# Performance work log

Hardware: AMD Instinct MI355X
Metric: run time of the kernel (lower is better)

The kernel has to match this reference:

```python
import jax, jax.numpy as jnp
import numpy as np

N = 50000      # n_nodes
E = 800000     # directed edges (symmetric set, no self-loops)
D_IN = 128
D_HID = 128
EPS = 1e-5     # LayerNorm eps (torch default)


def setup_inputs() -> dict:
    rng = np.random.default_rng(0)
    a = rng.integers(0, N, 700000, dtype=np.int64)
    b = rng.integers(0, N, 700000, dtype=np.int64)
    m = a != b
    a, b = a[m], b[m]
    # symmetric, deduplicated edge set (no self-loops); shuffle before truncation
    keys = np.unique(np.concatenate([a * N + b, b * N + a]))
    keys = rng.permutation(keys)[:E]
    row = (keys // N).astype(np.int32)
    col = (keys % N).astype(np.int32)
    ks = jax.random.split(jax.random.key(0), 6)
    return {
        "x": jax.random.normal(ks[0], (N, D_IN), jnp.float32),
        "W0": jax.random.normal(ks[1], (D_IN, D_HID), jnp.float32) / np.float32(np.sqrt(D_IN)),
        "b0": jnp.zeros((D_HID,), jnp.float32),
        "W1": jax.random.normal(ks[2], (D_HID, D_HID), jnp.float32) / np.float32(np.sqrt(D_HID)),
        "b1": jnp.zeros((D_HID,), jnp.float32),
        "ln1_g": jnp.ones((D_HID,), jnp.float32),
        "ln1_b": jnp.zeros((D_HID,), jnp.float32),
        "ln2_g": jnp.ones((D_HID,), jnp.float32),
        "ln2_b": jnp.zeros((D_HID,), jnp.float32),
        "drop_W": jax.random.normal(ks[3], (1, 2), jnp.float32) * 10.0,
        "drop_b": jnp.zeros((1,), jnp.float32),
        "row": jnp.asarray(row),
        "col": jnp.asarray(col),
    }


def _layernorm(h, g, b):
    mu = jnp.mean(h, axis=-1, keepdims=True)
    var = jnp.var(h, axis=-1, keepdims=True)
    return (h - mu) * jax.lax.rsqrt(var + EPS) * g + b


def _att_coef(h, row, col, drop_W, drop_b):
    # fused on-device version of the CPU att_coef: per-edge cosine sim,
    # threshold, row-l1-normalize, learned binary drop, self-loop lam, exp.
    n = h.shape[0]
    norms = jnp.sqrt(jnp.sum(h * h, axis=1))                      # [n]
    sim = jnp.sum(h[row] * h[col], axis=1) / (norms[row] * norms[col])  # [E]
    sim = jnp.where(sim < 0.1, 0.0, sim)
    rs = jax.ops.segment_sum(sim, row, num_segments=n)            # row l1 norms
    att = sim / jnp.where(rs[row] > 0, rs[row], 1.0)
    # reverse-edge lookup att[col,row] via sorted uint32 keys (n*n < 2**32)
    nn = jnp.uint32(n)
    keys = row.astype(jnp.uint32) * nn + col.astype(jnp.uint32)
    order = jnp.argsort(keys)
    sk = keys[order]
    rk = col.astype(jnp.uint32) * nn + row.astype(jnp.uint32)
    pos = jnp.clip(jnp.searchsorted(sk, rk), 0, keys.shape[0] - 1)
    att_rev = jnp.where(sk[pos] == rk, att[order[pos]], 0.0)
    # drop_learn: Linear(2,1) -> sigmoid -> Threshold(0.5,0) -> Threshold(-0.49,1)
    # net effect: binary mask = 1 if sigmoid(score) > 0.5 else 0
    score = jax.nn.sigmoid(att * drop_W[0, 0] + att_rev * drop_W[0, 1] + drop_b[0])
    att = att * (score > 0.5).astype(h.dtype)
    deg = jax.ops.segment_sum((att != 0).astype(h.dtype), row, num_segments=n)
    lam = 1.0 / (deg + 1.0)                                       # self-loop weight
    w_e = jnp.where(att != 0, jnp.exp(att), 0.0)                  # exp only on stored nnz
    w_diag = jnp.exp(lam)
    # original computes attention on CPU numpy -> detached from autograd
    return jax.lax.stop_gradient(w_e), jax.lax.stop_gradient(w_diag)


def _conv(h, w_e, w_diag, row, col, W, b):
    s = h @ W                                                      # [n, d_out]
    agg = jax.ops.segment_sum(w_e[:, None] * s[col], row, num_segments=h.shape[0])
    return agg + w_diag[:, None] * s + b


def reference(x, W0, b0, W1, b1, ln1_g, ln1_b, ln2_g, ln2_b, drop_W, drop_b, row, col):
    h = x
    # layer 0
    w_e, w_d = _att_coef(h, row, col, drop_W, drop_b)
    h = _conv(h, w_e, w_d, row, col, W0, b0)
    h = jax.nn.relu(_layernorm(h, ln1_g, ln1_b))   # dropout: eval mode -> identity
    # layer 1
    w_e, w_d = _att_coef(h, row, col, drop_W, drop_b)
    h = _conv(h, w_e, w_d, row, col, W1, b1)
    h = jax.nn.relu(_layernorm(h, ln2_g, ln2_b))
    # final block: source bug reuses the last loop conv (convs[-2] == W1,b1)
    w_e, w_d = _att_coef(h, row, col, drop_W, drop_b)
    h = _conv(h, w_e, w_d, row, col, W1, b1)
    return jax.nn.log_softmax(h, axis=-1)
```

## Files before the change

kernel.cpp:

```cpp
#include <hip/hip_runtime.h>
#include <hip/hip_bf16.h>

#define D 128
#define EPS 1e-5f
#define SCAP 32

__global__ __launch_bounds__(256) void k_pre(
    const int* __restrict__ row, int* __restrict__ cnt, int E,
    const float* __restrict__ h, float* __restrict__ nrm, int N, int cB) {
  if ((int)blockIdx.x < cB) {
    int e = blockIdx.x * 256 + threadIdx.x;
    if (e < E) atomicAdd(&cnt[row[e]], 1);
  } else {
    int i = (blockIdx.x - cB) * 8 + (threadIdx.x >> 5);
    int sub = threadIdx.x & 31;
    if (i >= N) return;
    float4 a = ((const float4*)(h + (size_t)i * D))[sub];
    float v = a.x * a.x + a.y * a.y + a.z * a.z + a.w * a.w;
    for (int off = 16; off > 0; off >>= 1) v += __shfl_down(v, off, 32);
    if (sub == 0) nrm[i] = sqrtf(v);
  }
}

__global__ __launch_bounds__(256) void k_bsum(const int* __restrict__ cnt,
                                              int* __restrict__ bsum) {
  int t = threadIdx.x;
  int base = blockIdx.x * 1024 + t * 4;
  int4 c4 = ((const int4*)(cnt + base))[0];
  int s = c4.x + c4.y + c4.z + c4.w;
  for (int off = 32; off > 0; off >>= 1) s += __shfl_down(s, off);
  __shared__ int sh[4];
  if ((t & 63) == 0) sh[t >> 6] = s;
  __syncthreads();
  if (t == 0) bsum[blockIdx.x] = sh[0] + sh[1] + sh[2] + sh[3];
}

__global__ __launch_bounds__(256) void k_bscan(const int* __restrict__ bsum,
                                               int* __restrict__ boff, int nb,
                                               int* __restrict__ rptr, int N, int E) {
  __shared__ int sh[256];
  int t = threadIdx.x;
  int v = (t < nb) ? bsum[t] : 0;
  sh[t] = v;
  __syncthreads();
  for (int off = 1; off < 256; off <<= 1) {
    int u = (t >= off) ? sh[t - off] : 0;
    __syncthreads();
    sh[t] += u;
    __syncthreads();
  }
  if (t < nb) boff[t] = sh[t] - v;
  if (t == 0) rptr[N] = E;
}

__global__ __launch_bounds__(256) void k_apply(const int* __restrict__ cnt,
                                               const int* __restrict__ boff,
                                               int* __restrict__ rptr, int N) {
  __shared__ int sh[256];
  int t = threadIdx.x;
  int base = blockIdx.x * 1024 + t * 4;
  int4 c4 = ((const int4*)(cnt + base))[0];
  int e1 = c4.x, e2 = c4.x + c4.y, e3 = c4.x + c4.y + c4.z;
  int tot = e3 + c4.w;
  sh[t] = tot;
  __syncthreads();
  for (int off = 1; off < 256; off <<= 1) {
    int u = (t >= off) ? sh[t - off] : 0;
    __syncthreads();
    sh[t] += u;
    __syncthreads();
  }
  int o = sh[t] - tot + boff[blockIdx.x];
  if (base + 0 < N) rptr[base + 0] = o;
  if (base + 1 < N) rptr[base + 1] = o + e1;
  if (base + 2 < N) rptr[base + 2] = o + e2;
  if (base + 3 < N) rptr[base + 3] = o + e3;
}

__global__ __launch_bounds__(256) void k_scatter(
    const int* __restrict__ row, const int* __restrict__ col,
    const int* __restrict__ rptr, int* __restrict__ cur,
    int* __restrict__ rowS, int* __restrict__ colS, int E) {
  int e = blockIdx.x * 256 + threadIdx.x;
  if (e < E) {
    int r = row[e];
    int p = rptr[r] + atomicAdd(&cur[r], 1);
    rowS[p] = r;
    colS[p] = col[e];
  }
}

__global__ __launch_bounds__(256) void k_rev(const int* __restrict__ rowS,
                                             const int* __restrict__ colS,
                                             const int* __restrict__ rptr,
                                             int* __restrict__ rev, int E) {
  int p = blockIdx.x * 256 + threadIdx.x;
  if (p >= E) return;
  int r = rowS[p], c = colS[p];
  int q1 = rptr[c + 1];
  int rv = -1;
  for (int q = rptr[c]; q < q1; ++q)
    if (colS[q] == r) { rv = q; break; }
  rev[p] = rv;
}

__global__ __launch_bounds__(256) void k_sim(
    const float* __restrict__ h, const float* __restrict__ nrm,
    const int* __restrict__ rptr, const int* __restrict__ colS,
    const int* __restrict__ rev, float* __restrict__ simS, int N) {
  __shared__ int cL[8 * SCAP];
  __shared__ int pL[8 * SCAP];
  __shared__ int rL[8 * SCAP];
  __shared__ float nL[8 * SCAP];
  int grp = threadIdx.x >> 5;
  int sub = threadIdx.x & 31;
  int half = grp & 1;
  int i = blockIdx.x * 8 + grp;
  if (i >= N) return;
  int gb = grp * SCAP;
  int p0 = rptr[i], p1 = rptr[i + 1];
  float4 ai = ((const float4*)(h + (size_t)i * D))[sub];
  float ni = nrm[i];
  for (int base = p0; base < p1; base += SCAP) {
    int p = base + sub;
    bool inr = p < p1;
    int c = inr ? colS[p] : 0;
    int rv = inr ? rev[p] : 0;
    bool ok = inr && (c > i || rv < 0);
    unsigned long long mb = __ballot(ok);
    unsigned mh = (unsigned)(mb >> (half * 32));
    int pos = __popc(mh & ((1u << sub) - 1u));
    int K = __popc(mh);
    if (ok) {
      cL[gb + pos] = c;
      pL[gb + pos] = p;
      rL[gb + pos] = rv;
      nL[gb + pos] = nrm[c];
    }
    __builtin_amdgcn_wave_barrier();
    for (int j0 = 0; j0 < K; j0 += 8) {
      int cc_[8];
      bool vv[8];
      float4 b[8];
#pragma unroll
      for (int k = 0; k < 8; ++k) {
        int idx = j0 + k;
        vv[k] = idx < K;
        cc_[k] = vv[k] ? cL[gb + idx] : i;
      }
#pragma unroll
      for (int k = 0; k < 8; ++k)
        b[k] = ((const float4*)(h + (size_t)cc_[k] * D))[sub];
#pragma unroll
      for (int k = 0; k < 8; ++k) {
        float v = ai.x * b[k].x + ai.y * b[k].y + ai.z * b[k].z + ai.w * b[k].w;
        for (int off = 16; off > 0; off >>= 1) v += __shfl_down(v, off, 32);
        if (sub == 0 && vv[k]) {
          int idx = j0 + k;
          float sm = v / (ni * nL[gb + idx]);
          sm = (sm < 0.1f) ? 0.0f : sm;
          simS[pL[gb + idx]] = sm;
          int rv2 = rL[gb + idx];
          if (rv2 >= 0) simS[rv2] = sm;
        }
      }
    }
    __builtin_amdgcn_wave_barrier();
  }
}

__global__ __launch_bounds__(256) void k_rs(const float* __restrict__ simS,
                                            const int* __restrict__ rptr,
                                            float* __restrict__ rsE, int N) {
  int i = blockIdx.x * 256 + threadIdx.x;
  if (i >= N) return;
  int p1 = rptr[i + 1];
  float rs = 0.f;
  for (int p = rptr[i]; p < p1; ++p) rs += simS[p];
  rsE[i] = (rs > 0.f) ? rs : 1.f;
}

__global__ __launch_bounds__(256) void k_gemm(const float* __restrict__ h,
                                              const float* __restrict__ W,
                                              float* __restrict__ S, int N) {
  __shared__ float Ws[64 * D];
  int t = threadIdx.x;
  int i0 = blockIdx.x * 64;
  int tx = t & 15, ty = t >> 4;
  int gi[4];
  bool vld[4];
#pragma unroll
  for (int r = 0; r < 4; ++r) {
    gi[r] = i0 + ty * 4 + r;
    vld[r] = gi[r] < N;
  }
  float acc[4][8] = {};
  for (int ph = 0; ph < 2; ++ph) {
    __syncthreads();
    for (int ch = 0; ch < 8; ++ch) {
      int q = t + 256 * ch;
      ((float4*)Ws)[q] = ((const float4*)(W + (size_t)ph * 64 * D))[q];
    }
    __syncthreads();
    for (int kk = 0; kk < 16; ++kk) {
      float4 a4[4];
#pragma unroll
      for (int r = 0; r < 4; ++r)
        a4[r] = vld[r] ? ((const float4*)(h + (size_t)gi[r] * D))[ph * 16 + kk]
                       : make_float4(0.f, 0.f, 0.f, 0.f);
      float4 b0[4], b1[4];
#pragma unroll
      for (int k = 0; k < 4; ++k) {
        b0[k] = ((const float4*)(Ws + (kk * 4 + k) * D))[tx];
        b1[k] = ((const float4*)(Ws + (kk * 4 + k) * D))[16 + tx];
      }
#pragma unroll
      for (int r = 0; r < 4; ++r) {
        float4 a = a4[r];
#pragma unroll
        for (int c = 0; c < 4; ++c) {
          acc[r][c] += a.x * (&b0[0].x)[c] + a.y * (&b0[1].x)[c] +
                       a.z * (&b0[2].x)[c] + a.w * (&b0[3].x)[c];
          acc[r][4 + c] += a.x * (&b1[0].x)[c] + a.y * (&b1[1].x)[c] +
                           a.z * (&b1[2].x)[c] + a.w * (&b1[3].x)[c];
        }
      }
    }
  }
#pragma unroll
  for (int r = 0; r < 4; ++r) {
    if (vld[r]) {
      ((float4*)(S + (size_t)gi[r] * D))[tx] =
          make_float4(acc[r][0], acc[r][1], acc[r][2], acc[r][3]);
      ((float4*)(S + (size_t)gi[r] * D))[16 + tx] =
          make_float4(acc[r][4], acc[r][5], acc[r][6], acc[r][7]);
    }
  }
}

template <int MODE>
__global__ __launch_bounds__(256) void k_combine(
    const float* __restrict__ s, const float* __restrict__ simS,
    const float* __restrict__ rsE, const int* __restrict__ rev,
    const int* __restrict__ rptr, const int* __restrict__ colS,
    const float* __restrict__ bias, const float* __restrict__ g,
    const float* __restrict__ be, const float* __restrict__ dWp,
    const float* __restrict__ dbp, float* __restrict__ outF,
    float* __restrict__ nrmOut, int N) {
  __shared__ float wL[8 * 32];
  __shared__ int cLd[8 * 32];
  int grp = threadIdx.x >> 5, sub = threadIdx.x & 31;
  int half = grp & 1;
  int i = blockIdx.x * 8 + grp;
  if (i >= N) return;
  int gb = grp * 32;
  float w0 = dWp[0], w1 = dWp[1], bd = dbp[0];
  int p0 = rptr[i], p1 = rptr[i + 1];
  float ri = rsE[i];
  float4 acc = make_float4(0.f, 0.f, 0.f, 0.f);
  int deg = 0;
  for (int base = p0; base < p1; base += 32) {
    int p = base + sub;
    bool inr = p < p1;
    float sm = inr ? simS[p] : 0.f;
    int c = inr ? colS[p] : 0;
    int rv = inr ? rev[p] : -1;
    bool keep = false;
    float a = 0.f;
    if (sm != 0.f) {
      a = sm / ri;
      float ar = (rv >= 0) ? sm / rsE[c] : 0.f;
      float x = a * w0 + ar * w1 + bd;
      float sc = (x >= 0.f) ? 1.f / (1.f + expf(-x)) : expf(x) / (1.f + expf(x));
      keep = sc > 0.5f;
    }
    unsigned long long mb = __ballot(keep);
    unsigned mh = (unsigned)(mb >> (half * 32));
    int pos = __popc(mh & ((1u << sub) - 1u));
    int K = __popc(mh);
    if (keep) {
      wL[gb + pos] = expf(a);
      cLd[gb + pos] = c;
    }
    __builtin_amdgcn_wave_barrier();
    deg += K;
    for (int j0 = 0; j0 < K; j0 += 8) {
      int cc_[8];
      float ww[8];
      float4 b[8];
#pragma unroll
      for (int k = 0; k < 8; ++k) {
        int idx = j0 + k;
        bool vv = idx < K;
        cc_[k] = vv ? cLd[gb + idx] : i;
        ww[k] = vv ? wL[gb + idx] : 0.f;
      }
#pragma unroll
      for (int k = 0; k < 8; ++k)
        b[k] = ((const float4*)(s + (size_t)cc_[k] * D))[sub];
#pragma unroll
      for (int k = 0; k < 8; ++k) {
        acc.x += ww[k] * b[k].x; acc.y += ww[k] * b[k].y;
        acc.z += ww[k] * b[k].z; acc.w += ww[k] * b[k].w;
      }
    }
    __builtin_amdgcn_wave_barrier();
  }
  float wd = expf(1.0f / (float)(deg + 1));
  float4 sv = ((const float4*)(s + (size_t)i * D))[sub];
  float4 bb = ((const float4*)bias)[sub];
  float4 v = make_float4(acc.x + wd * sv.x + bb.x, acc.y + wd * sv.y + bb.y,
                         acc.z + wd * sv.z + bb.z, acc.w + wd * sv.w + bb.w);
  if (MODE == 0) {
    float sm = v.x + v.y + v.z + v.w;
    for (int off = 16; off > 0; off >>= 1) sm += __shfl_down(sm, off, 32);
    float mu = __shfl(sm, 0, 32) * (1.f / 128.f);
    float4 dv = make_float4(v.x - mu, v.y - mu, v.z - mu, v.w - mu);
    float q = dv.x * dv.x + dv.y * dv.y + dv.z * dv.z + dv.w * dv.w;
    for (int off = 16; off > 0; off >>= 1) q += __shfl_down(q, off, 32);
    float var = __shfl(q, 0, 32) * (1.f / 128.f);
    float rstd = rsqrtf(var + EPS);
    float4 gg = ((const float4*)g)[sub];
    float4 eb = ((const float4*)be)[sub];
    float4 y = make_float4(fmaxf(dv.x * rstd * gg.x + eb.x, 0.f),
                           fmaxf(dv.y * rstd * gg.y + eb.y, 0.f),
                           fmaxf(dv.z * rstd * gg.z + eb.z, 0.f),
                           fmaxf(dv.w * rstd * gg.w + eb.w, 0.f));
    ((float4*)(outF + (size_t)i * D))[sub] = y;
    float q2 = y.x * y.x + y.y * y.y + y.z * y.z + y.w * y.w;
    for (int off = 16; off > 0; off >>= 1) q2 += __shfl_down(q2, off, 32);
    if (sub == 0) nrmOut[i] = sqrtf(q2);
  } else {
    float mx = fmaxf(fmaxf(v.x, v.y), fmaxf(v.z, v.w));
    for (int off = 16; off > 0; off >>= 1) mx = fmaxf(mx, __shfl_down(mx, off, 32));
    float m = __shfl(mx, 0, 32);
    float es = expf(v.x - m) + expf(v.y - m) + expf(v.z - m) + expf(v.w - m);
    for (int off = 16; off > 0; off >>= 1) es += __shfl_down(es, off, 32);
    float l = logf(__shfl(es, 0, 32)) + m;
    ((float4*)(outF + (size_t)i * D))[sub] =
        make_float4(v.x - l, v.y - l, v.z - l, v.w - l);
  }
}

extern "C" void kernel_launch(void* const* d_in, const int* in_sizes, int n_in,
                              void* d_out, int out_size, void* d_ws, size_t ws_size,
                              hipStream_t stream) {
  const float* x   = (const float*)d_in[0];
  const float* W0  = (const float*)d_in[1];
  const float* b0  = (const float*)d_in[2];
  const float* W1  = (const float*)d_in[3];
  const float* b1  = (const float*)d_in[4];
  const float* g1  = (const float*)d_in[5];
  const float* be1 = (const float*)d_in[6];
  const float* g2  = (const float*)d_in[7];
  const float* be2 = (const float*)d_in[8];
  const float* dW  = (const float*)d_in[9];
  const float* db  = (const float*)d_in[10];
  const int* row   = (const int*)d_in[11];
  const int* col   = (const int*)d_in[12];
  int N = in_sizes[0] / D;
  int E = in_sizes[11];
  float* out = (float*)d_out;

  float* base = (float*)d_ws;
  size_t off = 0;
  auto alloc = [&](size_t elems) {
    float* p = base + off;
    off += (elems + 3) & ~(size_t)3;
    return p;
  };
  size_t N128 = (size_t)N * D;
  int nb = (N + 1023) / 1024;
  int NpadS = nb * 1024;
  float* hA   = alloc(N128);
  float* hB   = alloc(N128);
  float* s    = alloc(N128);
  int*   rowS = (int*)alloc(E);
  int*   colS = (int*)alloc(E);
  int*   rev  = (int*)alloc(E);
  float* simS = alloc(E);
  int*   cc   = (int*)alloc((size_t)2 * NpadS);
  int*   cnt  = cc;
  int*   cur  = cc + NpadS;
  int*   rptr = (int*)alloc(N + 1);
  float* rsE  = alloc(N);
  float* nrm  = alloc(N);
  int*   bsum = (int*)alloc(nb);
  int*   boff = (int*)alloc(nb);
  (void)ws_size; (void)n_in; (void)out_size;

  int cB = (E + 255) / 256;
  int nB = (N + 7) / 8;
  int nG = (N + 63) / 64;
  int nSim = (N + 7) / 8;
  int nRs = (N + 255) / 256;
  int nC = (N + 7) / 8;

  hipMemsetAsync(cc, 0, (size_t)2 * NpadS * sizeof(int), stream);
  k_pre<<<cB + nB, 256, 0, stream>>>(row, cnt, E, x, nrm, N, cB);
  k_bsum<<<nb, 256, 0, stream>>>(cnt, bsum);
  k_bscan<<<1, 256, 0, stream>>>(bsum, boff, nb, rptr, N, E);
  k_apply<<<nb, 256, 0, stream>>>(cnt, boff, rptr, N);
  k_scatter<<<cB, 256, 0, stream>>>(row, col, rptr, cur, rowS, colS, E);
  k_rev<<<cB, 256, 0, stream>>>(rowS, colS, rptr, rev, E);

  auto layer = [&](const float* hin, float* hout, const float* Wf,
                   const float* bf, const float* gf, const float* bef,
                   float* nrmOut, int mode) {
    k_sim<<<nSim, 256, 0, stream>>>(hin, nrm, rptr, colS, rev, simS, N);
    k_rs<<<nRs, 256, 0, stream>>>(simS, rptr, rsE, N);
    k_gemm<<<nG, 256, 0, stream>>>(hin, Wf, s, N);
    if (mode == 0)
      k_combine<0><<<nC, 256, 0, stream>>>(s, simS, rsE, rev, rptr, colS, bf, gf,
                                           bef, dW, db, hout, nrmOut, N);
    else
      k_combine<1><<<nC, 256, 0, stream>>>(s, simS, rsE, rev, rptr, colS, bf, gf,
                                           bef, dW, db, hout, nullptr, N);
  };
  layer(x, hA, W0, b0, g1, be1, nrm, 0);
  layer(hA, hB, W1, b1, g2, be2, nrm, 0);
  layer(hB, out, W1, b1, nullptr, nullptr, nullptr, 1);
}
```

Measured before the change: 612.9 us.

## Merge similarity and GEMM kernels into one launch; drop rowS array

The per-edge cosine-similarity kernel and the dense h@W GEMM are combined into a single launch, with block index selecting the role, so both run concurrently instead of back to back. The reverse-edge search kernel now maps one 32-lane group per row, which removes the need for the sorted row array and its writes. The combined kernel always reserves 32KB of shared memory for the GEMM tile, even in similarity blocks, which may lower occupancy for the similarity part.

```diff
diff --git a/kernel.cpp b/kernel.cpp
--- a/kernel.cpp
+++ b/kernel.cpp
@@ -80,92 +80,151 @@
 __global__ __launch_bounds__(256) void k_scatter(
     const int* __restrict__ row, const int* __restrict__ col,
     const int* __restrict__ rptr, int* __restrict__ cur,
-    int* __restrict__ rowS, int* __restrict__ colS, int E) {
+    int* __restrict__ colS, int E) {
   int e = blockIdx.x * 256 + threadIdx.x;
   if (e < E) {
     int r = row[e];
     int p = rptr[r] + atomicAdd(&cur[r], 1);
-    rowS[p] = r;
     colS[p] = col[e];
   }
 }
 
-__global__ __launch_bounds__(256) void k_rev(const int* __restrict__ rowS,
-                                             const int* __restrict__ colS,
+__global__ __launch_bounds__(256) void k_rev(const int* __restrict__ colS,
                                              const int* __restrict__ rptr,
-                                             int* __restrict__ rev, int E) {
-  int p = blockIdx.x * 256 + threadIdx.x;
-  if (p >= E) return;
-  int r = rowS[p], c = colS[p];
-  int q1 = rptr[c + 1];
-  int rv = -1;
-  for (int q = rptr[c]; q < q1; ++q)
-    if (colS[q] == r) { rv = q; break; }
-  rev[p] = rv;
-}
-
-__global__ __launch_bounds__(256) void k_sim(
+                                             int* __restrict__ rev, int N) {
+  int grp = threadIdx.x >> 5, sub = threadIdx.x & 31;
+  int i = blockIdx.x * 8 + grp;
+  if (i >= N) return;
+  int p0 = rptr[i], p1 = rptr[i + 1];
+  for (int p = p0 + sub; p < p1; p += 32) {
+    int c = colS[p];
+    int q1 = rptr[c + 1];
+    int rv = -1;
+    for (int q = rptr[c]; q < q1; ++q)
+      if (colS[q] == i) { rv = q; break; }
+    rev[p] = rv;
+  }
+}
+
+__global__ __launch_bounds__(256) void k_simgemm(
     const float* __restrict__ h, const float* __restrict__ nrm,
     const int* __restrict__ rptr, const int* __restrict__ colS,
-    const int* __restrict__ rev, float* __restrict__ simS, int N) {
+    const int* __restrict__ rev, float* __restrict__ simS,
+    const float* __restrict__ W, float* __restrict__ S, int N, int nSim) {
+  __shared__ float Ws[64 * D];
   __shared__ int cL[8 * SCAP];
   __shared__ int pL[8 * SCAP];
   __shared__ int rL[8 * SCAP];
   __shared__ float nL[8 * SCAP];
-  int grp = threadIdx.x >> 5;
-  int sub = threadIdx.x & 31;
-  int half = grp & 1;
-  int i = blockIdx.x * 8 + grp;
-  if (i >= N) return;
-  int gb = grp * SCAP;
-  int p0 = rptr[i], p1 = rptr[i + 1];
-  float4 ai = ((const float4*)(h + (size_t)i * D))[sub];
-  float ni = nrm[i];
-  for (int base = p0; base < p1; base += SCAP) {
-    int p = base + sub;
-    bool inr = p < p1;
-    int c = inr ? colS[p] : 0;
-    int rv = inr ? rev[p] : 0;
-    bool ok = inr && (c > i || rv < 0);
-    unsigned long long mb = __ballot(ok);
-    unsigned mh = (unsigned)(mb >> (half * 32));
-    int pos = __popc(mh & ((1u << sub) - 1u));
-    int K = __popc(mh);
-    if (ok) {
-      cL[gb + pos] = c;
-      pL[gb + pos] = p;
-      rL[gb + pos] = rv;
-      nL[gb + pos] = nrm[c];
-    }
-    __builtin_amdgcn_wave_barrier();
-    for (int j0 = 0; j0 < K; j0 += 8) {
-      int cc_[8];
-      bool vv[8];
-      float4 b[8];
-#pragma unroll
-      for (int k = 0; k < 8; ++k) {
-        int idx = j0 + k;
-        vv[k] = idx < K;
-        cc_[k] = vv[k] ? cL[gb + idx] : i;
-      }
-#pragma unroll
-      for (int k = 0; k < 8; ++k)
-        b[k] = ((const float4*)(h + (size_t)cc_[k] * D))[sub];
-#pragma unroll
-      for (int k = 0; k < 8; ++k) {
-        float v = ai.x * b[k].x + ai.y * b[k].y + ai.z * b[k].z + ai.w * b[k].w;
-        for (int off = 16; off > 0; off >>= 1) v += __shfl_down(v, off, 32);
-        if (sub == 0 && vv[k]) {
+  if ((int)blockIdx.x < nSim) {
+    int grp = threadIdx.x >> 5;
+    int sub = threadIdx.x & 31;
+    int half = grp & 1;
+    int i = blockIdx.x * 8 + grp;
+    if (i >= N) return;
+    int gb = grp * SCAP;
+    int p0 = rptr[i], p1 = rptr[i + 1];
+    float4 ai = ((const float4*)(h + (size_t)i * D))[sub];
+    float ni = nrm[i];
+    for (int base = p0; base < p1; base += SCAP) {
+      int p = base + sub;
+      bool inr = p < p1;
+      int c = inr ? colS[p] : 0;
+      int rv = inr ? rev[p] : 0;
+      bool ok = inr && (c > i || rv < 0);
+      unsigned long long mb = __ballot(ok);
+      unsigned mh = (unsigned)(mb >> (half * 32));
+      int pos = __popc(mh & ((1u << sub) - 1u));
+      int K = __popc(mh);
+      if (ok) {
+        cL[gb + pos] = c;
+        pL[gb + pos] = p;
+        rL[gb + pos] = rv;
+        nL[gb + pos] = nrm[c];
+      }
+      __builtin_amdgcn_wave_barrier();
+      for (int j0 = 0; j0 < K; j0 += 8) {
+        int cc_[8];
+        bool vv[8];
+        float4 b[8];
+#pragma unroll
+        for (int k = 0; k < 8; ++k) {
           int idx = j0 + k;
-          float sm = v / (ni * nL[gb + idx]);
-          sm = (sm < 0.1f) ? 0.0f : sm;
-          simS[pL[gb + idx]] = sm;
-          int rv2 = rL[gb + idx];
-          if (rv2 >= 0) simS[rv2] = sm;
+          vv[k] = idx < K;
+          cc_[k] = vv[k] ? cL[gb + idx] : i;
         }
-      }
-    }
-    __builtin_amdgcn_wave_barrier();
+#pragma unroll
+        for (int k = 0; k < 8; ++k)
+          b[k] = ((const float4*)(h + (size_t)cc_[k] * D))[sub];
+#pragma unroll
+        for (int k = 0; k < 8; ++k) {
+          float v = ai.x * b[k].x + ai.y * b[k].y + ai.z * b[k].z + ai.w * b[k].w;
+          for (int off = 16; off > 0; off >>= 1) v += __shfl_down(v, off, 32);
+          if (sub == 0 && vv[k]) {
+            int idx = j0 + k;
+            float sm = v / (ni * nL[gb + idx]);
+            sm = (sm < 0.1f) ? 0.0f : sm;
+            simS[pL[gb + idx]] = sm;
+            int rv2 = rL[gb + idx];
+            if (rv2 >= 0) simS[rv2] = sm;
+          }
+        }
+      }
+      __builtin_amdgcn_wave_barrier();
+    }
+  } else {
+    int t = threadIdx.x;
+    int i0 = ((int)blockIdx.x - nSim) * 64;
+    int tx = t & 15, ty = t >> 4;
+    int gi[4];
+    bool vld[4];
+#pragma unroll
+    for (int r = 0; r < 4; ++r) {
+      gi[r] = i0 + ty * 4 + r;
+      vld[r] = gi[r] < N;
+    }
+    float acc[4][8] = {};
+    for (int ph = 0; ph < 2; ++ph) {
+      __syncthreads();
+      for (int ch = 0; ch < 8; ++ch) {
+        int q = t + 256 * ch;
+        ((float4*)Ws)[q] = ((const float4*)(W + (size_t)ph * 64 * D))[q];
+      }
+      __syncthreads();
+      for (int kk = 0; kk < 16; ++kk) {
+        float4 a4[4];
+#pragma unroll
+        for (int r = 0; r < 4; ++r)
+          a4[r] = vld[r] ? ((const float4*)(h + (size_t)gi[r] * D))[ph * 16 + kk]
+                         : make_float4(0.f, 0.f, 0.f, 0.f);
+        float4 b0[4], b1[4];
+#pragma unroll
+        for (int k = 0; k < 4; ++k) {
+          b0[k] = ((const float4*)(Ws + (kk * 4 + k) * D))[tx];
+          b1[k] = ((const float4*)(Ws + (kk * 4 + k) * D))[16 + tx];
+        }
+#pragma unroll
+        for (int r = 0; r < 4; ++r) {
+          float4 a = a4[r];
+#pragma unroll
+          for (int c = 0; c < 4; ++c) {
+            acc[r][c] += a.x * (&b0[0].x)[c] + a.y * (&b0[1].x)[c] +
+                         a.z * (&b0[2].x)[c] + a.w * (&b0[3].x)[c];
+            acc[r][4 + c] += a.x * (&b1[0].x)[c] + a.y * (&b1[1].x)[c] +
+                             a.z * (&b1[2].x)[c] + a.w * (&b1[3].x)[c];
+          }
+        }
+      }
+    }
+#pragma unroll
+    for (int r = 0; r < 4; ++r) {
+      if (vld[r]) {
+        ((float4*)(S + (size_t)gi[r] * D))[tx] =
+            make_float4(acc[r][0], acc[r][1], acc[r][2], acc[r][3]);
+        ((float4*)(S + (size_t)gi[r] * D))[16 + tx] =
+            make_float4(acc[r][4], acc[r][5], acc[r][6], acc[r][7]);
+      }
+    }
   }
 }
 
@@ -178,64 +237,6 @@
   float rs = 0.f;
   for (int p = rptr[i]; p < p1; ++p) rs += simS[p];
   rsE[i] = (rs > 0.f) ? rs : 1.f;
-}
-
-__global__ __launch_bounds__(256) void k_gemm(const float* __restrict__ h,
-                                              const float* __restrict__ W,
-                                              float* __restrict__ S, int N) {
-  __shared__ float Ws[64 * D];
-  int t = threadIdx.x;
-  int i0 = blockIdx.x * 64;
-  int tx = t & 15, ty = t >> 4;
-  int gi[4];
-  bool vld[4];
-#pragma unroll
-  for (int r = 0; r < 4; ++r) {
-    gi[r] = i0 + ty * 4 + r;
-    vld[r] = gi[r] < N;
-  }
-  float acc[4][8] = {};
-  for (int ph = 0; ph < 2; ++ph) {
-    __syncthreads();
-    for (int ch = 0; ch < 8; ++ch) {
-      int q = t + 256 * ch;
-      ((float4*)Ws)[q] = ((const float4*)(W + (size_t)ph * 64 * D))[q];
-    }
-    __syncthreads();
-    for (int kk = 0; kk < 16; ++kk) {
-      float4 a4[4];
-#pragma unroll
-      for (int r = 0; r < 4; ++r)
-        a4[r] = vld[r] ? ((const float4*)(h + (size_t)gi[r] * D))[ph * 16 + kk]
-                       : make_float4(0.f, 0.f, 0.f, 0.f);
-      float4 b0[4], b1[4];
-#pragma unroll
-      for (int k = 0; k < 4; ++k) {
-        b0[k] = ((const float4*)(Ws + (kk * 4 + k) * D))[tx];
-        b1[k] = ((const float4*)(Ws + (kk * 4 + k) * D))[16 + tx];
-      }
-#pragma unroll
-      for (int r = 0; r < 4; ++r) {
-        float4 a = a4[r];
-#pragma unroll
-        for (int c = 0; c < 4; ++c) {
-          acc[r][c] += a.x * (&b0[0].x)[c] + a.y * (&b0[1].x)[c] +
-                       a.z * (&b0[2].x)[c] + a.w * (&b0[3].x)[c];
-          acc[r][4 + c] += a.x * (&b1[0].x)[c] + a.y * (&b1[1].x)[c] +
-                           a.z * (&b1[2].x)[c] + a.w * (&b1[3].x)[c];
-        }
-      }
-    }
-  }
-#pragma unroll
-  for (int r = 0; r < 4; ++r) {
-    if (vld[r]) {
-      ((float4*)(S + (size_t)gi[r] * D))[tx] =
-          make_float4(acc[r][0], acc[r][1], acc[r][2], acc[r][3]);
-      ((float4*)(S + (size_t)gi[r] * D))[16 + tx] =
-          make_float4(acc[r][4], acc[r][5], acc[r][6], acc[r][7]);
-    }
-  }
 }
 
 template <int MODE>
@@ -375,7 +376,6 @@
   float* hA   = alloc(N128);
   float* hB   = alloc(N128);
   float* s    = alloc(N128);
-  int*   rowS = (int*)alloc(E);
   int*   colS = (int*)alloc(E);
   int*   rev  = (int*)alloc(E);
   float* simS = alloc(E);
@@ -401,15 +401,15 @@
   k_bsum<<<nb, 256, 0, stream>>>(cnt, bsum);
   k_bscan<<<1, 256, 0, stream>>>(bsum, boff, nb, rptr, N, E);
   k_apply<<<nb, 256, 0, stream>>>(cnt, boff, rptr, N);
-  k_scatter<<<cB, 256, 0, stream>>>(row, col, rptr, cur, rowS, colS, E);
-  k_rev<<<cB, 256, 0, stream>>>(rowS, colS, rptr, rev, E);
+  k_scatter<<<cB, 256, 0, stream>>>(row, col, rptr, cur, colS, E);
+  k_rev<<<nSim, 256, 0, stream>>>(colS, rptr, rev, N);
 
   auto layer = [&](const float* hin, float* hout, const float* Wf,
                    const float* bf, const float* gf, const float* bef,
                    float* nrmOut, int mode) {
-    k_sim<<<nSim, 256, 0, stream>>>(hin, nrm, rptr, colS, rev, simS, N);
+    k_simgemm<<<nSim + nG, 256, 0, stream>>>(hin, nrm, rptr, colS, rev, simS,
+                                             Wf, s, N, nSim);
     k_rs<<<nRs, 256, 0, stream>>>(simS, rptr, rsE, N);
-    k_gemm<<<nG, 256, 0, stream>>>(hin, Wf, s, N);
     if (mode == 0)
       k_combine<0><<<nC, 256, 0, stream>>>(s, simS, rsE, rev, rptr, colS, bf, gf,
                                            bef, dW, db, hout, nrmOut, N);
```

Result: no change. 621.3 us (+1.4%).
